# Optimization experiments

Measured on AMD Instinct MI355X. Metric: run time of the kernel, lower is better.

## Reference

```python
import jax, jax.numpy as jnp
import numpy as np

B, S, H, NH = 8, 1024, 1024, 16
HD = H // NH


def setup_inputs() -> dict:
    key = jax.random.key(0)
    ks = jax.random.split(key, 9)
    scale = 0.02
    d = {"x": jax.random.normal(ks[0], (B, S, H), jnp.float32)}
    for i, n in enumerate(["q", "k", "v", "o"]):
        d["W" + n] = jax.random.normal(ks[1 + i], (H, H), jnp.float32) * scale
        d["b" + n] = jnp.zeros((H,), jnp.float32)
    d["position_idx"] = jnp.arange(S, dtype=jnp.int32).reshape(1, S)
    return d


def _rotate_half(x):
    x1, x2 = jnp.split(x, 2, axis=-1)
    return jnp.concatenate([-x2, x1], axis=-1)


def _apply_rope(x, position_idx):
    # Faithful to source (precedence bug included): (10000**arange) / head_dim
    inv_freq = 1.0 / (10000.0 ** jnp.arange(0, HD, 2, dtype=jnp.float32) / HD)
    freqs = jnp.einsum('bi,j->bij', position_idx.astype(jnp.float32), inv_freq)  # [1,S,HD/2]
    emb = jnp.concatenate([freqs, freqs], axis=-1)  # [1,S,HD]
    cos = jnp.cos(emb).reshape(1, 1, -1, HD)
    sin = jnp.sin(emb).reshape(1, 1, -1, HD)
    return x * cos + _rotate_half(x) * sin


def reference(x, Wq, bq, Wk, bk, Wv, bv, Wo, bo, position_idx):
    b, s, _ = x.shape

    def to_heads(t):  # [b,s,H] -> [b,nh,s,hd]
        return t.reshape(b, s, NH, HD).transpose(0, 2, 1, 3)

    q = to_heads(x @ Wq + bq)
    k = to_heads(x @ Wk + bk)
    v = to_heads(x @ Wv + bv)
    q = _apply_rope(q, position_idx)
    k = _apply_rope(k, position_idx)
    scores = jnp.einsum('bhqd,bhkd->bhqk', q, k) / jnp.sqrt(jnp.float32(HD))
    attn = jax.nn.softmax(scores, axis=-1)
    out = jnp.einsum('bhqk,bhkd->bhqd', attn, v)  # [b,nh,s,hd]
    out = out.transpose(0, 2, 1, 3).reshape(b, s, NH * HD)
    return out @ Wo + bo
```

## Files before the change

kernel.cpp:

```cpp
#include <hip/hip_runtime.h>
#include <hip/hip_bf16.h>
#include <math.h>

#define B_  8
#define S_  1024
#define H_  1024
#define NH_ 16
#define HD_ 64
#define M_  (B_*S_)
#define K_  1024

typedef __hip_bfloat16 bf16;
typedef __attribute__((ext_vector_type(8))) short  short8;
typedef __attribute__((ext_vector_type(4))) short  short4v;
typedef __attribute__((ext_vector_type(8))) __bf16 bf16x8;
typedef __attribute__((ext_vector_type(4))) float  f32x4;

#define MFMA16(a, b, c) __builtin_amdgcn_mfma_f32_16x16x32_bf16((a), (b), (c), 0, 0, 0)
#define QSCALE 0.18033688011112042f

static __device__ __forceinline__ short f2bf_s(float f) {
  unsigned u = __float_as_uint(f);
  u += 0x7fffu + ((u >> 16) & 1u);
  return (short)(u >> 16);
}
static __device__ __forceinline__ float bf2f_s(short s) {
  return __uint_as_float((unsigned)(unsigned short)s << 16);
}

static __device__ __forceinline__ void gload16(const void* g, void* l) {
  __builtin_amdgcn_global_load_lds(
      (const __attribute__((address_space(1))) void*)g,
      (__attribute__((address_space(3))) void*)l, 16, 0, 0);
}

__global__ void prepA_kernel(const int* __restrict__ pos,
                             float* __restrict__ cost, float* __restrict__ sint,
                             const float* __restrict__ b0, const float* __restrict__ b1,
                             const float* __restrict__ b2, const float* __restrict__ b3,
                             short* __restrict__ bbuf) {
  if (blockIdx.x < 128) {
    int i = blockIdx.x * 256 + threadIdx.x;
    int s = i >> 5, f = i & 31;
    double inv = 64.0 / pow(10000.0, (double)(2 * f));
    double ang = (double)pos[s] * inv;
    cost[i] = (float)cos(ang);
    sint[i] = (float)sin(ang);
  } else {
    int i = (blockIdx.x - 128) * 256 + threadIdx.x;
    const float* src = (i < 1024) ? b0 : (i < 2048) ? b1 : (i < 3072) ? b2 : b3;
    bbuf[i] = f2bf_s(src[i & 1023]);
  }
}

__global__ __launch_bounds__(256) void prepB_kernel(
    const float* __restrict__ x, short* __restrict__ xb,
    const float* __restrict__ w0, const float* __restrict__ w1,
    const float* __restrict__ w2, const float* __restrict__ w3,
    bf16* __restrict__ outbase) {
  __shared__ short tile[64][72];
  const int t = threadIdx.x;
  if (blockIdx.x < 4096) {
    int i = blockIdx.x * 256 + t;
    size_t base = (size_t)i * 8;
    f32x4 a = *(const f32x4*)(x + base);
    f32x4 b = *(const f32x4*)(x + base + 4);
    short8 v;
    #pragma unroll
    for (int j = 0; j < 4; ++j) { v[j] = f2bf_s(a[j]); v[4 + j] = f2bf_s(b[j]); }
    *(short8*)(xb + base) = v;
    return;
  }
  int tw = blockIdx.x - 4096;
  int wsel = tw >> 8, ti = tw & 255;
  const float* src = (wsel == 0) ? w0 : (wsel == 1) ? w1 : (wsel == 2) ? w2 : w3;
  short* dst = (short*)outbase + (size_t)wsel * H_ * H_;
  const int tr = ti >> 4, tc = ti & 15;
  const int r0 = tr * 64, c0 = tc * 64;
  #pragma unroll
  for (int p = 0; p < 2; ++p) {
    int row = p * 32 + (t >> 3);
    int c8  = (t & 7) * 8;
    const float* f = src + (size_t)(r0 + row) * H_ + c0 + c8;
    #pragma unroll
    for (int j = 0; j < 8; ++j) tile[c8 + j][row] = f2bf_s(f[j]);
  }
  __syncthreads();
  #pragma unroll
  for (int p = 0; p < 2; ++p) {
    int row = p * 32 + (t >> 3);
    int c8  = (t & 7) * 8;
    short8 v;
    #pragma unroll
    for (int j = 0; j < 8; ++j) v[j] = tile[row][c8 + j];
    *(short8*)(dst + (size_t)(c0 + row) * H_ + r0 + c8) = v;
  }
}

__global__ __launch_bounds__(256) void gemm_bt_kernel(
    const bf16* __restrict__ A, const bf16* __restrict__ Bt, const short* __restrict__ bias,
    void* __restrict__ C, const float* __restrict__ cost, const float* __restrict__ sint,
    int mode, float qscale) {
  __shared__ short sA[2][128 * 64];
  __shared__ short sB[2][128 * 64];
  const int t  = threadIdx.x;
  const int bm = blockIdx.x * 128, bn = blockIdx.y * 128;
  const int lane = t & 63, wid = t >> 6;
  const int wr = wid >> 1, wc = wid & 1;
  const int lm = lane & 15, lg = lane >> 4;
  f32x4 acc[4][4] = {};

  const short* Ag = (const short*)A;
  const short* Bg = (const short*)Bt;

  #pragma unroll
  for (int c = 0; c < 4; ++c) {
    int flat = c * 256 + t;
    int row = flat >> 3, cc = flat & 7;
    int gcol = (cc ^ (row & 7)) * 8;
    gload16(Ag + (size_t)(bm + row) * K_ + gcol, sA[0] + flat * 8);
    gload16(Bg + (size_t)(bn + row) * K_ + gcol, sB[0] + flat * 8);
  }
  __syncthreads();

  int cur = 0;
  for (int k0 = 0; k0 < K_; k0 += 64) {
    if (k0 + 64 < K_) {
      #pragma unroll
      for (int c = 0; c < 4; ++c) {
        int flat = c * 256 + t;
        int row = flat >> 3, cc = flat & 7;
        int gcol = (cc ^ (row & 7)) * 8;
        gload16(Ag + (size_t)(bm + row) * K_ + k0 + 64 + gcol, sA[cur ^ 1] + flat * 8);
        gload16(Bg + (size_t)(bn + row) * K_ + k0 + 64 + gcol, sB[cur ^ 1] + flat * 8);
      }
    }
    const short* sAc = sA[cur];
    const short* sBc = sB[cur];
    #pragma unroll
    for (int kk2 = 0; kk2 < 2; ++kk2) {
      bf16x8 af[4], bfr[4];
      #pragma unroll
      for (int i = 0; i < 4; ++i) {
        int row = wr * 64 + i * 16 + lm;
        af[i] = *(const bf16x8*)(sAc + row * 64 + (((kk2 << 2) + lg) ^ (row & 7)) * 8);
      }
      #pragma unroll
      for (int j = 0; j < 4; ++j) {
        int row = wc * 64 + j * 16 + lm;
        bfr[j] = *(const bf16x8*)(sBc + row * 64 + (((kk2 << 2) + lg) ^ (row & 7)) * 8);
      }
      #pragma unroll
      for (int i = 0; i < 4; ++i)
        #pragma unroll
        for (int j = 0; j < 4; ++j)
          acc[i][j] = MFMA16(af[i], bfr[j], acc[i][j]);
    }
    __syncthreads();
    cur ^= 1;
  }

  if (mode == 0) {
    #pragma unroll
    for (int i = 0; i < 4; ++i) {
      int row = bm + wr * 64 + i * 16 + lg * 4;
      #pragma unroll
      for (int j = 0; j < 4; ++j) {
        int col = bn + wc * 64 + j * 16 + lm;
        float bv = bf2f_s(bias[col]);
        #pragma unroll
        for (int r = 0; r < 4; ++r)
          ((float*)C)[(size_t)(row + r) * H_ + col] = acc[i][j][r] + bv;
      }
    }
  } else if (mode == 1) {
    #pragma unroll
    for (int i = 0; i < 4; ++i) {
      int row = bm + wr * 64 + i * 16 + lg * 4;
      #pragma unroll
      for (int j = 0; j < 2; ++j) {
        int col0 = bn + wc * 64 + j * 16 + lm;
        int d = col0 & 63;
        float b0 = bf2f_s(bias[col0]);
        float b1 = bf2f_s(bias[col0 + 32]);
        #pragma unroll
        for (int r = 0; r < 4; ++r) {
          int s = (row + r) & (S_ - 1);
          float cv = cost[s * 32 + d] * qscale, sv = sint[s * 32 + d] * qscale;
          float x1 = acc[i][j][r] + b0;
          float x2 = acc[i][j + 2][r] + b1;
          ((short*)C)[(size_t)(row + r) * H_ + col0]      = f2bf_s(x1 * cv - x2 * sv);
          ((short*)C)[(size_t)(row + r) * H_ + col0 + 32] = f2bf_s(x2 * cv + x1 * sv);
        }
      }
    }
  } else {
    #pragma unroll
    for (int i = 0; i < 4; ++i) {
      int row = bm + wr * 64 + i * 16 + lg * 4;
      int bb = row >> 10;
      int sb = row & 1023;
      int pos = (sb & ~31) | (((sb >> 2) & 3) << 3) | (((sb >> 4) & 1) << 2);
      #pragma unroll
      for (int j = 0; j < 4; ++j) {
        int col = bn + wc * 64 + j * 16 + lm;
        int colv = col & 1023;
        float bv = bf2f_s(bias[col]);
        short4v pk;
        #pragma unroll
        for (int r = 0; r < 4; ++r) pk[r] = f2bf_s(acc[i][j][r] + bv);
        short* dstp = (short*)C + ((size_t)(bb * NH_ + (colv >> 6)) * HD_ + (colv & 63)) * S_ + pos;
        *(short4v*)dstp = pk;
      }
    }
  }
}

__global__ __launch_bounds__(128) void attn_kernel(
    const bf16* __restrict__ q, const bf16* __restrict__ k,
    const bf16* __restrict__ vt, bf16* __restrict__ o) {
  const int bh = blockIdx.x, b = bh >> 4, h = bh & 15;
  const int t = threadIdx.x, wid = t >> 6, lane = t & 63;
  const int lm = lane & 15, lg = lane >> 4;
  const int qw = blockIdx.y * 128 + wid * 64;

  __shared__ short sK[2][32 * 64];
  __shared__ short sV[2][64 * 32];

  const short* srcBase;
  if (wid == 0) {
    int keyr = lane >> 3, cc = lane & 7;
    srcBase = (const short*)k + (size_t)(b * S_ + keyr) * H_ + h * HD_ + ((cc ^ (keyr & 7)) * 8);
  } else {
    int dr = lane >> 2, cc = lane & 3;
    srcBase = (const short*)vt + (size_t)bh * HD_ * S_ + (size_t)dr * S_ + ((cc ^ (dr & 3)) * 8);
  }

  const int kO0 = lm * 64 + ((lg ^ (lm & 7)) << 3);
  const int kO1 = lm * 64 + (((4 + lg) ^ (lm & 7)) << 3);
  const int vO  = lm * 32 + ((lg ^ (lm & 3)) << 3);

  const short* qbase = (const short*)q + (size_t)(b * S_ + qw) * H_ + h * HD_;
  bf16x8 qf[4][2];
  #pragma unroll
  for (int mi = 0; mi < 4; ++mi)
    #pragma unroll
    for (int dh = 0; dh < 2; ++dh)
      qf[mi][dh] = *(const bf16x8*)(qbase + (size_t)(mi * 16 + lm) * H_ + dh * 32 + lg * 8);

  bf16x8 ones;
  #pragma unroll
  for (int j = 0; j < 8; ++j) ones[j] = (__bf16)1.0f;

  f32x4 sacc[4] = {};
  f32x4 oacc[4][4] = {};

  if (wid == 0) {
    #pragma unroll
    for (int i = 0; i < 4; ++i)
      gload16(srcBase + (size_t)i * 8 * H_, sK[0] + i * 512 + lane * 8);
  } else {
    #pragma unroll
    for (int i = 0; i < 4; ++i)
      gload16(srcBase + (size_t)i * 16 * S_, sV[0] + i * 512 + lane * 8);
  }
  __syncthreads();

  int cur = 0;
  for (int kk = 0; kk < S_; kk += 32) {
    if (kk + 32 < S_) {
      if (wid == 0) {
        #pragma unroll
        for (int i = 0; i < 4; ++i)
          gload16(srcBase + (size_t)(kk + 32) * H_ + (size_t)i * 8 * H_,
                  sK[cur ^ 1] + i * 512 + lane * 8);
      } else {
        #pragma unroll
        for (int i = 0; i < 4; ++i)
          gload16(srcBase + (kk + 32) + (size_t)i * 16 * S_,
                  sV[cur ^ 1] + i * 512 + lane * 8);
      }
    }
    const short* sKc = sK[cur];
    const short* sVc = sV[cur];

    f32x4 sc[4][2];
    __builtin_amdgcn_s_setprio(1);
    #pragma unroll
    for (int nt = 0; nt < 2; ++nt) {
      bf16x8 kf0 = *(const bf16x8*)(sKc + nt * 16 * 64 + kO0);
      bf16x8 kf1 = *(const bf16x8*)(sKc + nt * 16 * 64 + kO1);
      #pragma unroll
      for (int mi = 0; mi < 4; ++mi) {
        f32x4 z = {};
        z = MFMA16(kf0, qf[mi][0], z);
        sc[mi][nt] = MFMA16(kf1, qf[mi][1], z);
      }
    }
    __builtin_amdgcn_s_setprio(0);
    bf16x8 vf[4];
    #pragma unroll
    for (int dt = 0; dt < 4; ++dt)
      vf[dt] = *(const bf16x8*)(sVc + dt * 16 * 32 + vO);

    bf16x8 pf[4];
    #pragma unroll
    for (int mi = 0; mi < 4; ++mi)
      #pragma unroll
      for (int nt = 0; nt < 2; ++nt)
        #pragma unroll
        for (int r = 0; r < 4; ++r)
          pf[mi][nt * 4 + r] = (__bf16)exp2f(sc[mi][nt][r]);

    __builtin_amdgcn_s_setprio(1);
    #pragma unroll
    for (int mi = 0; mi < 4; ++mi) {
      sacc[mi] = MFMA16(pf[mi], ones, sacc[mi]);
      #pragma unroll
      for (int dt = 0; dt < 4; ++dt)
        oacc[mi][dt] = MFMA16(pf[mi], vf[dt], oacc[mi][dt]);
    }
    __builtin_amdgcn_s_setprio(0);

    __syncthreads();
    cur ^= 1;
  }
  #pragma unroll
  for (int mi = 0; mi < 4; ++mi) {
    #pragma unroll
    for (int r = 0; r < 4; ++r) {
      float rr = 1.0f / sacc[mi][r];
      int row = qw + mi * 16 + lg * 4 + r;
      #pragma unroll
      for (int dt = 0; dt < 4; ++dt) {
        int col = h * HD_ + dt * 16 + lm;
        ((short*)o)[(size_t)(b * S_ + row) * H_ + col] = f2bf_s(oacc[mi][dt][r] * rr);
      }
    }
  }
}

extern "C" void kernel_launch(void* const* d_in, const int* in_sizes, int n_in,
                              void* d_out, int out_size, void* d_ws, size_t ws_size,
                              hipStream_t stream) {
  (void)out_size; (void)ws_size;
  int ix, iWq, iWk, iWv, iWo, ibq, ibk, ibv, ibo, ipos;
  const int XS = 8388608, WS = 1048576;
  if (n_in == 10 && in_sizes[0] == WS && in_sizes[9] == XS) {
    iWk = 0; iWo = 1; iWq = 2; iWv = 3; ibk = 4; ibo = 5; ibq = 6; ibv = 7; ipos = 8; ix = 9;
  } else if (n_in == 10 && in_sizes[0] == 1024 && in_sizes[9] == XS) {
    ipos = 0; ibo = 1; iWo = 2; ibv = 3; iWv = 4; ibk = 5; iWk = 6; ibq = 7; iWq = 8; ix = 9;
  } else if (n_in == 10 && in_sizes[0] == XS && in_sizes[1] == 1024) {
    ix = 0; ipos = 1; ibv = 2; ibq = 3; ibo = 4; ibk = 5; iWv = 6; iWq = 7; iWo = 8; iWk = 9;
  } else {
    ix = 0; iWq = 1; ibq = 2; iWk = 3; ibk = 4; iWv = 5; ibv = 6; iWo = 7; ibo = 8; ipos = 9;
  }
  const float* x  = (const float*)d_in[ix];
  const float* Wq = (const float*)d_in[iWq];
  const float* bq = (const float*)d_in[ibq];
  const float* Wk = (const float*)d_in[iWk];
  const float* bk = (const float*)d_in[ibk];
  const float* Wv = (const float*)d_in[iWv];
  const float* bv = (const float*)d_in[ibv];
  const float* Wo = (const float*)d_in[iWo];
  const float* bo = (const float*)d_in[ibo];
  const int*  pos = (const int*)d_in[ipos];

  char* ws = (char*)d_ws;
  bf16* wt    = (bf16*)(ws);
  bf16* kb    = (bf16*)(ws + (8ull  << 20));
  bf16* vtb   = (bf16*)(ws + (24ull << 20));
  bf16* obuf  = (bf16*)(ws + (40ull << 20));
  float* cost = (float*)(ws + (40ull << 20));
  float* sint = (float*)(ws + (40ull << 20) + (size_t)S_ * 32 * sizeof(float));
  short* bbuf = (short*)(ws + (56ull << 20));
  bf16* qb    = (bf16*)d_out;
  short* xb   = (short*)((char*)d_out + (16ull << 20));

  const int NEL = H_ * H_;
  prepA_kernel<<<dim3(144), 256, 0, stream>>>(pos, cost, sint, bq, bk, bv, bo, bbuf);
  prepB_kernel<<<dim3(5120), 256, 0, stream>>>(x, xb, Wq, Wk, Wv, Wo, wt);
  gemm_bt_kernel<<<dim3(64, 8), 256, 0, stream>>>((const bf16*)xb, wt + 0 * NEL, bbuf + 0,
                                                  qb,  cost, sint, 1, QSCALE);
  gemm_bt_kernel<<<dim3(64, 8), 256, 0, stream>>>((const bf16*)xb, wt + 1 * NEL, bbuf + 1024,
                                                  kb,  cost, sint, 1, 1.0f);
  gemm_bt_kernel<<<dim3(64, 8), 256, 0, stream>>>((const bf16*)xb, wt + 2 * NEL, bbuf + 2048,
                                                  vtb, cost, sint, 2, 1.0f);
  attn_kernel<<<dim3(128, 8), 128, 0, stream>>>(qb, kb, vtb, obuf);
  gemm_bt_kernel<<<dim3(64, 8), 256, 0, stream>>>(obuf, wt + 3 * NEL, bbuf + 3072,
                                                  d_out, cost, sint, 0, 1.0f);
}
```

Measured before the change: 166.1 us.

## Split attention over two key halves with a separate reduction kernel

Each attention block now processes half the key sequence, doubling the grid to improve CU occupancy. Unnormalized partial outputs and row sums are written to scratch buffers, and a new reduce kernel adds the halves and normalizes. This adds extra global traffic and a kernel launch, and stores unnormalized partials in bf16.

```diff
diff --git a/kernel.cpp b/kernel.cpp
--- a/kernel.cpp
+++ b/kernel.cpp
@@ -218,11 +218,14 @@
 
 __global__ __launch_bounds__(128) void attn_kernel(
     const bf16* __restrict__ q, const bf16* __restrict__ k,
-    const bf16* __restrict__ vt, bf16* __restrict__ o) {
+    const bf16* __restrict__ vt, bf16* __restrict__ p0, bf16* __restrict__ p1,
+    float* __restrict__ sums) {
   const int bh = blockIdx.x, b = bh >> 4, h = bh & 15;
+  const int ky = blockIdx.y >> 3, qc = blockIdx.y & 7;
   const int t = threadIdx.x, wid = t >> 6, lane = t & 63;
   const int lm = lane & 15, lg = lane >> 4;
-  const int qw = blockIdx.y * 128 + wid * 64;
+  const int qw = qc * 128 + wid * 64;
+  const int kbase0 = ky * 512;
 
   __shared__ short sK[2][32 * 64];
   __shared__ short sV[2][64 * 32];
@@ -230,10 +233,12 @@
   const short* srcBase;
   if (wid == 0) {
     int keyr = lane >> 3, cc = lane & 7;
-    srcBase = (const short*)k + (size_t)(b * S_ + keyr) * H_ + h * HD_ + ((cc ^ (keyr & 7)) * 8);
+    srcBase = (const short*)k + (size_t)(b * S_ + kbase0 + keyr) * H_ + h * HD_
+              + ((cc ^ (keyr & 7)) * 8);
   } else {
     int dr = lane >> 2, cc = lane & 3;
-    srcBase = (const short*)vt + (size_t)bh * HD_ * S_ + (size_t)dr * S_ + ((cc ^ (dr & 3)) * 8);
+    srcBase = (const short*)vt + (size_t)bh * HD_ * S_ + (size_t)dr * S_ + kbase0
+              + ((cc ^ (dr & 3)) * 8);
   }
 
   const int kO0 = lm * 64 + ((lg ^ (lm & 7)) << 3);
@@ -267,8 +272,8 @@
   __syncthreads();
 
   int cur = 0;
-  for (int kk = 0; kk < S_; kk += 32) {
-    if (kk + 32 < S_) {
+  for (int kk = 0; kk < 512; kk += 32) {
+    if (kk + 32 < 512) {
       if (wid == 0) {
         #pragma unroll
         for (int i = 0; i < 4; ++i)
@@ -325,19 +330,39 @@
     __syncthreads();
     cur ^= 1;
   }
+  bf16* po = ky ? p1 : p0;
   #pragma unroll
   for (int mi = 0; mi < 4; ++mi) {
     #pragma unroll
     for (int r = 0; r < 4; ++r) {
-      float rr = 1.0f / sacc[mi][r];
       int row = qw + mi * 16 + lg * 4 + r;
+      if (lm == 0)
+        sums[(size_t)ky * 131072 + (size_t)(b * 1024 + row) * 16 + h] = sacc[mi][r];
       #pragma unroll
       for (int dt = 0; dt < 4; ++dt) {
         int col = h * HD_ + dt * 16 + lm;
-        ((short*)o)[(size_t)(b * S_ + row) * H_ + col] = f2bf_s(oacc[mi][dt][r] * rr);
-      }
-    }
-  }
+        ((short*)po)[(size_t)(b * S_ + row) * H_ + col] = f2bf_s(oacc[mi][dt][r]);
+      }
+    }
+  }
+}
+
+__global__ __launch_bounds__(256) void attn_reduce_kernel(
+    const bf16* __restrict__ p0, const bf16* __restrict__ p1,
+    const float* __restrict__ sums, bf16* __restrict__ obuf) {
+  int i = blockIdx.x * 256 + threadIdx.x;
+  size_t base = (size_t)i * 8;
+  int R = (int)(base >> 10);
+  int h = ((int)(base & 1023)) >> 6;
+  float s = sums[(size_t)R * 16 + h] + sums[131072 + (size_t)R * 16 + h];
+  float rr = 1.0f / s;
+  short8 a = *(const short8*)((const short*)p0 + base);
+  short8 c = *(const short8*)((const short*)p1 + base);
+  short8 o;
+  #pragma unroll
+  for (int j = 0; j < 8; ++j)
+    o[j] = f2bf_s((bf2f_s(a[j]) + bf2f_s(c[j])) * rr);
+  *(short8*)((short*)obuf + base) = o;
 }
 
 extern "C" void kernel_launch(void* const* d_in, const int* in_sizes, int n_in,
@@ -374,8 +399,10 @@
   float* cost = (float*)(ws + (40ull << 20));
   float* sint = (float*)(ws + (40ull << 20) + (size_t)S_ * 32 * sizeof(float));
   short* bbuf = (short*)(ws + (56ull << 20));
+  float* sums = (float*)(ws);
   bf16* qb    = (bf16*)d_out;
   short* xb   = (short*)((char*)d_out + (16ull << 20));
+  bf16* part1 = (bf16*)((char*)d_out + (16ull << 20));
 
   const int NEL = H_ * H_;
   prepA_kernel<<<dim3(144), 256, 0, stream>>>(pos, cost, sint, bq, bk, bv, bo, bbuf);
@@ -386,7 +413,8 @@
                                                   kb,  cost, sint, 1, 1.0f);
   gemm_bt_kernel<<<dim3(64, 8), 256, 0, stream>>>((const bf16*)xb, wt + 2 * NEL, bbuf + 2048,
                                                   vtb, cost, sint, 2, 1.0f);
-  attn_kernel<<<dim3(128, 8), 128, 0, stream>>>(qb, kb, vtb, obuf);
+  attn_kernel<<<dim3(128, 16), 128, 0, stream>>>(qb, kb, vtb, obuf, part1, sums);
+  attn_reduce_kernel<<<dim3(4096), 256, 0, stream>>>(obuf, part1, sums, obuf);
   gemm_bt_kernel<<<dim3(64, 8), 256, 0, stream>>>(obuf, wt + 3 * NEL, bbuf + 3072,
                                                   d_out, cost, sint, 0, 1.0f);
 }
```

After: 193.5 us. 16.5% more time.
